# Kernel optimization log

Hardware: AMD Instinct MI355X
Metric: run time of the kernel (lower is better)

The kernel has to match this reference:

```python
import jax, jax.numpy as jnp
import numpy as np

B = 32768          # rays
N = 512            # gaussians
NSH = 4            # -> m = 2*NSH+1 = 9 SH coeffs
H = 512.0
W = 512.0
S_MIN = 1.0 / 30.0       # 1 / n_gaussian_max_pixels
S_MAX = 1.0 / 0.75       # 1 / n_gaussian_min_pixels
MU_BORDER = 1.05
PI_APPROX = 3.1416       # matches the literal in the torch source


def setup_inputs() -> dict:
    key = jax.random.key(0)
    ks = jax.random.split(key, 6)
    # pixel coordinates in [0, W) x [0, H)
    x = jax.random.uniform(ks[0], (B, 2), jnp.float32) * jnp.array([W, H], jnp.float32)
    rgbsh = jax.random.uniform(ks[1], (N, 2 * NSH + 1, 3), jnp.float32)
    opacity = jax.random.uniform(ks[2], (N,), jnp.float32)
    mu = jax.random.uniform(ks[3], (N, 2), jnp.float32) * 2.0 - 1.0
    scale = jax.random.uniform(ks[4], (N, 2), jnp.float32)
    angle = jax.random.uniform(ks[5], (N,), jnp.float32) * 2.0 - 1.0
    return {"x": x, "rgbsh": rgbsh, "opacity": opacity,
            "mu": mu, "scale": scale, "angle": angle}


def _forward(x, rgbsh, opacity, mu, scale, angle):
    wh = jnp.array([W, H], x.dtype)                      # (2,)
    xnorm = x / wh * 2.0 - 1.0                           # (B,2) in [-1,1]
    gmu = jnp.tanh(mu) * MU_BORDER                       # (N,2)
    S = jnp.clip(scale, 0.0, 1.0) * (S_MAX - S_MIN) + S_MIN  # (N,2) inverse radii

    # pixel-space offset ray->gaussian: (x - mu)/2 * (w,h)
    vec = (xnorm[:, None, :] - gmu[None, :, :]) * (wh * 0.5)   # (B,N,2)

    # validity mask (computed under no_grad in torch): |S * vec| < 5
    dist = jnp.linalg.norm(vec * S[None], axis=-1)             # (B,N)
    valid = jax.lax.stop_gradient(dist < 5.0)

    # per-gaussian rotation matrices
    alpha = jnp.tanh(angle) * PI_APPROX                        # (N,)
    c, s = jnp.cos(alpha), jnp.sin(alpha)
    R = jnp.stack([jnp.stack([c, -s], -1),
                   jnp.stack([s,  c], -1)], axis=-2)           # (N,2,2)

    # Mahalanobis-like squared distance: || R @ diag(S) @ vec ||^2
    svec = vec * S[None]                                       # (B,N,2)
    rot = jnp.einsum('nij,bnj->bni', R, svec)                  # (B,N,2)
    d2 = jnp.sum(rot * rot, axis=-1)                           # (B,N)

    # view angle in the gaussian frame
    vnorm = vec / (1e-10 + jnp.linalg.norm(vec, axis=-1, keepdims=True))
    vrot = jnp.einsum('nij,bnj->bni', R, vnorm)                # (B,N,2)
    theta = jnp.arctan2(vrot[..., 0], vrot[..., 1])            # (B,N)

    # 2D SH basis: [1, sin(t), cos(t), sin(2t), cos(2t), ...]
    basis = [jnp.ones_like(theta)]
    for i in range(NSH):
        basis.append(jnp.sin(theta * (i + 1)))
        basis.append(jnp.cos(theta * (i + 1)))
    basis = jnp.stack(basis, axis=-1)                          # (B,N,M)

    rgb = jax.nn.sigmoid(jnp.einsum('bnm,nmc->bnc', basis, rgbsh))  # (B,N,3)
    wgt = jnp.where(valid,
                    jnp.exp(-d2) * jax.nn.sigmoid(opacity)[None, :],
                    jnp.zeros((), x.dtype))                    # (B,N)

    # accumulate_along_rays: per-ray weighted sum over gaussians
    return jnp.einsum('bn,bnc->bc', wgt, rgb)                  # (B,3)


def reference(x, rgbsh, opacity, mu, scale, angle):
    return _forward(x, rgbsh, opacity, mu, scale, angle)
```

## Files before the change

kernel.cpp:

```cpp
#include <hip/hip_runtime.h>

#define BDIM 1024
#define NW   16
#define RPB  64
#define NG   512
#define GPW  (NG / NW)
#define QCAP 256


__global__ void pre_kernel(const float* __restrict__ rgbsh,
                           const float* __restrict__ opacity,
                           const float* __restrict__ mu,
                           const float* __restrict__ scale,
                           const float* __restrict__ angle,
                           float4* __restrict__ wsA,
                           float*  __restrict__ wsH,
                           int N)
{
    int n = blockIdx.x * blockDim.x + threadIdx.x;
    if (n >= N) return;
    const float S_MIN = 1.0f / 30.0f;
    const float S_MAX = 1.0f / 0.75f;
    float gmx = tanhf(mu[2 * n + 0]) * 1.05f;
    float gmy = tanhf(mu[2 * n + 1]) * 1.05f;
    float Sx = fminf(fmaxf(scale[2 * n + 0], 0.0f), 1.0f) * (S_MAX - S_MIN) + S_MIN;
    float Sy = fminf(fmaxf(scale[2 * n + 1], 0.0f), 1.0f) * (S_MAX - S_MIN) + S_MIN;
    float ax = 256.0f * Sx, ay = 256.0f * Sy;
    wsA[n] = make_float4(ax, ay, -gmx * ax, -gmy * ay);
    float a = tanhf(angle[n]) * 3.1416f;
    float sa, ca;
    sincosf(a, &sa, &ca);
    float* hp = wsH + ((size_t)n << 5);
    hp[0] = ca;
    hp[1] = sa;
    hp[2] = 1.0f / (1.0f + expf(-opacity[n]));
    hp[3] = 1.0f / Sx;
    hp[4] = 1.0f / Sy;
    #pragma unroll
    for (int q = 0; q < 27; ++q) hp[5 + q] = rgbsh[n * 27 + q];
}

__global__ __launch_bounds__(BDIM, 8) void splat_kernel(
    const float*  __restrict__ x,
    const float4* __restrict__ wsA,
    const float*  __restrict__ wsH,
    float* __restrict__ out,
    int B)
{
    __shared__ float acc[NW][RPB * 3];
    __shared__ float pn[2][RPB];
    __shared__ unsigned short queue[NW][QCAP];
    const int tid  = threadIdx.x;
    const int lane = tid & 63;
    const int w = __builtin_amdgcn_readfirstlane(tid >> 6);

    const int b  = blockIdx.x * RPB + lane;
    const int bb = (b < B) ? b : (B - 1);
    float2 p2 = *(const float2*)(x + 2 * bb);
    float pnx = p2.x * (1.0f / 256.0f) - 1.0f;
    float pny = p2.y * (1.0f / 256.0f) - 1.0f;

    if (w == 0) { pn[0][lane] = pnx; pn[1][lane] = pny; }
    #pragma unroll
    for (int c = 0; c < 3; ++c) acc[w][lane * 3 + c] = 0.0f;
    __syncthreads();

    const int g0 = w * GPW;
    const float4* __restrict__ wA = wsA + g0;

    int qlen = 0;

    auto flush = [&]() {
        for (int qi = lane; qi < qlen; qi += 64) {
            const int e  = queue[w][qi];
            const int l  = e & 63;
            const int g  = g0 + (e >> 6);
            const float qx = pn[0][l];
            const float qy = pn[1][l];
            const float4 pa = wsA[g];
            const float sx = fmaf(qx, pa.x, pa.z);
            const float sy = fmaf(qy, pa.y, pa.w);
            const float4* hp = (const float4*)(wsH + ((size_t)g << 5));
            const float4 f0 = hp[0], f1 = hp[1], f2 = hp[2], f3 = hp[3];
            const float4 f4 = hp[4], f5 = hp[5], f6 = hp[6], f7 = hp[7];
            const float c = f0.x, s = f0.y, w0 = f0.z, iSx = f0.w, iSy = f1.x;
            float rx = fmaf(c, sx, -s * sy);
            float ry = fmaf(s, sx,  c * sy);
            float d2 = fmaf(rx, rx, ry * ry);
            float vx  = sx * iSx;
            float vy  = sy * iSy;
            float len = sqrtf(fmaf(vx, vx, vy * vy));
            float inv = __builtin_amdgcn_rcpf(1e-10f + len);
            float rvx = fmaf(c, vx, -s * vy);
            float rvy = fmaf(s, vx,  c * vy);
            float s1 = rvx * inv, c1 = rvy * inv;
            float s2 = 2.0f * s1 * c1;
            float c2 = fmaf(c1, c1, -s1 * s1);
            float s3 = fmaf(s2, c1,  c2 * s1);
            float c3 = fmaf(c2, c1, -s2 * s1);
            float s4 = 2.0f * s2 * c2;
            float c4 = fmaf(c2, c2, -s2 * s2);
            float rr = f1.y, gg = f1.z, bb2 = f1.w;
            rr = fmaf(s1, f2.x, rr);  gg = fmaf(s1, f2.y, gg);  bb2 = fmaf(s1, f2.z, bb2);
            rr = fmaf(c1, f2.w, rr);  gg = fmaf(c1, f3.x, gg);  bb2 = fmaf(c1, f3.y, bb2);
            rr = fmaf(s2, f3.z, rr);  gg = fmaf(s2, f3.w, gg);  bb2 = fmaf(s2, f4.x, bb2);
            rr = fmaf(c2, f4.y, rr);  gg = fmaf(c2, f4.z, gg);  bb2 = fmaf(c2, f4.w, bb2);
            rr = fmaf(s3, f5.x, rr);  gg = fmaf(s3, f5.y, gg);  bb2 = fmaf(s3, f5.z, bb2);
            rr = fmaf(c3, f5.w, rr);  gg = fmaf(c3, f6.x, gg);  bb2 = fmaf(c3, f6.y, bb2);
            rr = fmaf(s4, f6.z, rr);  gg = fmaf(s4, f6.w, gg);  bb2 = fmaf(s4, f7.x, bb2);
            rr = fmaf(c4, f7.y, rr);  gg = fmaf(c4, f7.z, gg);  bb2 = fmaf(c4, f7.w, bb2);
            rr  = __builtin_amdgcn_rcpf(1.0f + __expf(-rr));
            gg  = __builtin_amdgcn_rcpf(1.0f + __expf(-gg));
            bb2 = __builtin_amdgcn_rcpf(1.0f + __expf(-bb2));
            float wt = __expf(-d2) * w0;
            atomicAdd(&acc[w][l * 3 + 0], wt * rr);
            atomicAdd(&acc[w][l * 3 + 1], wt * gg);
            atomicAdd(&acc[w][l * 3 + 2], wt * bb2);
        }
        qlen = 0;
    };

    #pragma unroll 2
    for (int j = 0; j < GPW; ++j) {
        float4 pa = wA[j];
        float sx = fmaf(pnx, pa.x, pa.z);
        float sy = fmaf(pny, pa.y, pa.w);
        float t  = fmaf(sx, sx, sy * sy);
        bool  v  = t < 25.0f;
        unsigned long long mask = __ballot(v);
        if (mask) {
            int prefix = __popcll(mask & ((1ull << lane) - 1ull));
            if (v) queue[w][qlen + prefix] = (unsigned short)((j << 6) | lane);
            qlen += __popcll(mask);
            if (qlen > QCAP - 64) flush();
        }
    }
    flush();

    __syncthreads();
    if (tid < RPB * 3) {
        float s = 0.0f;
        #pragma unroll
        for (int w2 = 0; w2 < NW; ++w2)
            s += acc[w2][tid];
        const int idx = blockIdx.x * (RPB * 3) + tid;
        if (idx < 3 * B)
            out[idx] = s;
    }
}

extern "C" void kernel_launch(void* const* d_in, const int* in_sizes, int n_in,
                              void* d_out, int out_size, void* d_ws, size_t ws_size,
                              hipStream_t stream) {
    const float* x       = (const float*)d_in[0];
    const float* rgbsh   = (const float*)d_in[1];
    const float* opacity = (const float*)d_in[2];
    const float* mu      = (const float*)d_in[3];
    const float* scale   = (const float*)d_in[4];
    const float* angle   = (const float*)d_in[5];
    float* out = (float*)d_out;

    const int B = in_sizes[0] / 2;
    const int N = in_sizes[2];

    char* ws = (char*)d_ws;
    float4* wsA = (float4*)(ws);
    float*  wsH = (float*)(ws + (size_t)N * 16);

    pre_kernel<<<(N + 255) / 256, 256, 0, stream>>>(rgbsh, opacity, mu, scale,
                                                    angle, wsA, wsH, N);
    splat_kernel<<<(B + RPB - 1) / RPB, BDIM, 0, stream>>>(x, wsA, wsH, out, B);
}
```

Baseline: 72.86 us.

## Transpose culling loop: lanes own gaussians, iterate rays via readlane

The culling scan is transposed. Each lane now holds one gaussian in registers and the loop walks the 64 rays of the block, broadcasting each ray's coordinates with readlane, so the per-iteration global loads of gaussian parameters go away. Block size drops to 8 waves of 64 gaussians each, with the occupancy hint lowered to 4. Ray coordinates in the flush step are fetched with ds_bpermute instead of a shared-memory array, and the flush loop is padded to full wavefronts so every lane takes part in the permute. This adds a fully unrolled 64-iteration loop and masked atomics, and it fixes GPW at 64, which only covers all 512 gaussians together with NW=8.

```diff
diff --git a/kernel.cpp b/kernel.cpp
--- a/kernel.cpp
+++ b/kernel.cpp
@@ -1,10 +1,10 @@
 #include <hip/hip_runtime.h>
 
-#define BDIM 1024
-#define NW   16
+#define BDIM 512
+#define NW   8
 #define RPB  64
 #define NG   512
-#define GPW  (NG / NW)
+#define GPW  64
 #define QCAP 256
 
 
@@ -40,7 +40,7 @@
     for (int q = 0; q < 27; ++q) hp[5 + q] = rgbsh[n * 27 + q];
 }
 
-__global__ __launch_bounds__(BDIM, 8) void splat_kernel(
+__global__ __launch_bounds__(BDIM, 4) void splat_kernel(
     const float*  __restrict__ x,
     const float4* __restrict__ wsA,
     const float*  __restrict__ wsH,
@@ -48,38 +48,43 @@
     int B)
 {
     __shared__ float acc[NW][RPB * 3];
-    __shared__ float pn[2][RPB];
     __shared__ unsigned short queue[NW][QCAP];
     const int tid  = threadIdx.x;
     const int lane = tid & 63;
     const int w = __builtin_amdgcn_readfirstlane(tid >> 6);
 
+    const int   gid = w * GPW + lane;
+    const float4 pa = wsA[gid];
+
     const int b  = blockIdx.x * RPB + lane;
     const int bb = (b < B) ? b : (B - 1);
     float2 p2 = *(const float2*)(x + 2 * bb);
-    float pnx = p2.x * (1.0f / 256.0f) - 1.0f;
-    float pny = p2.y * (1.0f / 256.0f) - 1.0f;
+    const float pnx = p2.x * (1.0f / 256.0f) - 1.0f;
+    const float pny = p2.y * (1.0f / 256.0f) - 1.0f;
+    const int ipnx = __builtin_bit_cast(int, pnx);
+    const int ipny = __builtin_bit_cast(int, pny);
 
-    if (w == 0) { pn[0][lane] = pnx; pn[1][lane] = pny; }
     #pragma unroll
     for (int c = 0; c < 3; ++c) acc[w][lane * 3 + c] = 0.0f;
     __syncthreads();
 
-    const int g0 = w * GPW;
-    const float4* __restrict__ wA = wsA + g0;
-
     int qlen = 0;
 
     auto flush = [&]() {
-        for (int qi = lane; qi < qlen; qi += 64) {
-            const int e  = queue[w][qi];
-            const int l  = e & 63;
-            const int g  = g0 + (e >> 6);
-            const float qx = pn[0][l];
-            const float qy = pn[1][l];
-            const float4 pa = wsA[g];
-            const float sx = fmaf(qx, pa.x, pa.z);
-            const float sy = fmaf(qy, pa.y, pa.w);
+        const int qtot = (qlen + 63) & ~63;
+        for (int qi = lane; qi < qtot; qi += 64) {
+            const bool live = (qi < qlen);
+            const int e  = live ? (int)queue[w][qi] : 0;
+            const int r  = e >> 6;
+            const int gl = e & 63;
+            const float qx = __builtin_bit_cast(float,
+                __builtin_amdgcn_ds_bpermute(r << 2, ipnx));
+            const float qy = __builtin_bit_cast(float,
+                __builtin_amdgcn_ds_bpermute(r << 2, ipny));
+            const int g = w * GPW + gl;
+            const float4 pb = wsA[g];
+            const float sx = fmaf(qx, pb.x, pb.z);
+            const float sy = fmaf(qy, pb.y, pb.w);
             const float4* hp = (const float4*)(wsH + ((size_t)g << 5));
             const float4 f0 = hp[0], f1 = hp[1], f2 = hp[2], f3 = hp[3];
             const float4 f4 = hp[4], f5 = hp[5], f6 = hp[6], f7 = hp[7];
@@ -113,24 +118,29 @@
             gg  = __builtin_amdgcn_rcpf(1.0f + __expf(-gg));
             bb2 = __builtin_amdgcn_rcpf(1.0f + __expf(-bb2));
             float wt = __expf(-d2) * w0;
-            atomicAdd(&acc[w][l * 3 + 0], wt * rr);
-            atomicAdd(&acc[w][l * 3 + 1], wt * gg);
-            atomicAdd(&acc[w][l * 3 + 2], wt * bb2);
+            if (live) {
+                atomicAdd(&acc[w][r * 3 + 0], wt * rr);
+                atomicAdd(&acc[w][r * 3 + 1], wt * gg);
+                atomicAdd(&acc[w][r * 3 + 2], wt * bb2);
+            }
         }
         qlen = 0;
     };
 
-    #pragma unroll 2
-    for (int j = 0; j < GPW; ++j) {
-        float4 pa = wA[j];
-        float sx = fmaf(pnx, pa.x, pa.z);
-        float sy = fmaf(pny, pa.y, pa.w);
+    #pragma unroll
+    for (int r = 0; r < RPB; ++r) {
+        const float spx = __builtin_bit_cast(float,
+            __builtin_amdgcn_readlane(ipnx, r));
+        const float spy = __builtin_bit_cast(float,
+            __builtin_amdgcn_readlane(ipny, r));
+        float sx = fmaf(spx, pa.x, pa.z);
+        float sy = fmaf(spy, pa.y, pa.w);
         float t  = fmaf(sx, sx, sy * sy);
         bool  v  = t < 25.0f;
         unsigned long long mask = __ballot(v);
         if (mask) {
             int prefix = __popcll(mask & ((1ull << lane) - 1ull));
-            if (v) queue[w][qlen + prefix] = (unsigned short)((j << 6) | lane);
+            if (v) queue[w][qlen + prefix] = (unsigned short)((r << 6) | lane);
             qlen += __popcll(mask);
             if (qlen > QCAP - 64) flush();
         }
```

New measurement: 72.10 us. No clear change (-1.0%).
